# Kernel tuning notes

Measured on AMD Instinct MI355X. Metric: run time of the kernel, lower is better.

The kernel has to match this reference:

```python
import jax, jax.numpy as jnp
import numpy as np

B, N, D = 4, 10000, 64
C, E = 2, 160000  # adj channels, edges per (graph, channel)
EPS = 1e-10


def setup_inputs() -> dict:
    key = jax.random.key(0)
    k1, k2, k3 = jax.random.split(key, 3)
    inputs = jax.random.normal(k1, (B, N, D), dtype=jnp.float32)
    edge_idx = jax.random.randint(k2, (B, C, E, 2), 0, N, dtype=jnp.int32)
    weight_a = 0.1 * jax.random.normal(k3, (C, 2 * D, 1), dtype=jnp.float32)
    return {"inputs": inputs, "edge_idx": edge_idx, "weight_a": weight_a}


def _gat_channel(x, idx, wa):
    # x: [N, D], idx: [E, 2] (col 0 = scatter/dst node, col 1 = gather/src node), wa: [2D, 1]
    n = x.shape[0]
    a1 = x[idx[:, 1]]                      # [E, D]
    a2 = x[idx[:, 0]]                      # [E, D]
    score = jnp.concatenate([a1, a2], axis=1) @ wa   # [E, 1]
    e = jnp.exp(jax.nn.leaky_relu(score, negative_slope=0.2))  # [E, 1]
    denom = jax.ops.segment_sum(e, idx[:, 0], num_segments=n)  # [N, 1]  (ii @ e)
    denom_e = denom[idx[:, 1]]             # [E, 1]  (faithful to original: gather by idx[:,1])
    alpha = e / (denom_e + EPS)            # [E, 1]
    r = jax.ops.segment_sum(alpha * a1, idx[:, 0], num_segments=n)  # [N, D]
    return jax.nn.sigmoid(r)


def _gat_graph(x, idx_all, weight_a):
    # x: [N, D], idx_all: [C, E, 2], weight_a: [C, 2D, 1]
    per_ch = jax.vmap(_gat_channel, in_axes=(None, 0, 0))(x, idx_all, weight_a)  # [C, N, D]
    return per_ch.sum(axis=0)


def reference(inputs, edge_idx, weight_a):
    # inputs: [B, N, D], edge_idx: [B, C, E, 2], weight_a: [C, 2D, 1]
    return jax.vmap(_gat_graph, in_axes=(0, 0, None))(inputs, edge_idx, weight_a)
```

## Files before the change

### kernel.cpp

```cpp
#include <hip/hip_runtime.h>

#define B_ 4
#define N_ 10000
#define D_ 64
#define C_ 2
#define E_ 160000
#define BC_ (B_ * C_)
#define SH2_ 7
#define NB2_ 128
#define G2_ 79
#define CAPF_ 2560
#define NBLK_ 125
#define EPT_ 5
#define EPB_ (256 * EPT_)
#define YBLK_ (BC_ * 40)
#define POISON_ 0xAAAAAAAAu
#define EPS_ 1e-10f

__global__ void gat_yb(const float* __restrict__ x, const float* __restrict__ wa,
                       float* __restrict__ y1, float* __restrict__ y0,
                       const int* __restrict__ eidx, int* __restrict__ gcount,
                       unsigned int* __restrict__ bpack) {
    int tid = threadIdx.x;
    if (blockIdx.x < YBLK_) {
        int bc = blockIdx.x & 7;
        int n  = (blockIdx.x >> 3) * 256 + tid;
        if (n >= N_) return;
        int b = bc / C_, c = bc % C_;
        const float4* xr = (const float4*)(x + ((size_t)b * N_ + n) * D_);
        const float4* w1 = (const float4*)(wa + (size_t)c * 2 * D_);
        const float4* w0 = w1 + D_ / 4;
        float a = 0.f, bb = 0.f;
#pragma unroll
        for (int i = 0; i < D_ / 4; ++i) {
            float4 xv = xr[i];
            float4 u = w1[i], v = w0[i];
            a  += xv.x * u.x + xv.y * u.y + xv.z * u.z + xv.w * u.w;
            bb += xv.x * v.x + xv.y * v.y + xv.z * v.z + xv.w * v.w;
        }
        y1[bc * N_ + n] = a;
        y0[bc * N_ + n] = bb;
        return;
    }
    int bid = blockIdx.x - YBLK_;
    int bc  = bid & 7;
    int blk = bid >> 3;
    const int2* ep = (const int2*)eidx + (size_t)bc * E_ + (size_t)blk * EPB_;
    __shared__ int sd[128];
    __shared__ int excl[G2_], cur[G2_], gbase[G2_];
    __shared__ unsigned int stage[EPB_];
    if (tid < 128) sd[tid] = 0;
    __syncthreads();
    unsigned int pk[EPT_];
    int gg[EPT_];
#pragma unroll
    for (int k = 0; k < EPT_; ++k) {
        int2 v = ep[k * 256 + tid];
        int g  = v.x >> SH2_;
        gg[k]  = g;
        pk[k]  = ((unsigned int)g << 21) |
                 ((unsigned int)(v.x & (NB2_ - 1)) << 14) |
                 (unsigned int)v.y;
        atomicAdd(&sd[g], 1);
    }
    __syncthreads();
    int cnt = (tid < 128) ? sd[tid] : 0;
    for (int off = 1; off < 128; off <<= 1) {
        int t = (tid < 128 && tid >= off) ? sd[tid - off] : 0;
        __syncthreads();
        if (tid < 128) sd[tid] += t;
        __syncthreads();
    }
    if (tid < G2_) {
        int ex = sd[tid] - cnt;
        excl[tid]  = ex;
        cur[tid]   = ex;
        unsigned int ret = (unsigned int)atomicAdd(&gcount[bc * G2_ + tid], cnt);
        gbase[tid] = (int)(ret - POISON_);
    }
    __syncthreads();
#pragma unroll
    for (int k = 0; k < EPT_; ++k) {
        int slot = atomicAdd(&cur[gg[k]], 1);
        stage[slot] = pk[k];
    }
    __syncthreads();
#pragma unroll
    for (int k = 0; k < EPT_; ++k) {
        int idx = k * 256 + tid;
        unsigned int p = stage[idx];
        int g     = p >> 21;
        int local = idx - excl[g];
        bpack[((size_t)bc * G2_ + g) * CAPF_ + gbase[g] + local] =
            (((p >> 14) & 127u) << 16) | (p & 16383u);
    }
}

__global__ void gat_fine(const unsigned int* __restrict__ bpack,
                         const int* __restrict__ gcount,
                         const float* __restrict__ y1, const float* __restrict__ y0,
                         unsigned short* __restrict__ csr_i1,
                         int* __restrict__ rs_s, int* __restrict__ rs_e,
                         float2* __restrict__ yrd) {
    int bc = blockIdx.x & 7;
    int g  = blockIdx.x >> 3;
    int K  = (int)((unsigned int)gcount[bc * G2_ + g] - POISON_);
    int R  = (bc * G2_ + g) * CAPF_;
    const unsigned int* bp = bpack + R;
    const float* y1p = y1 + bc * N_;
    int tid = threadIdx.x;

    __shared__ int   cnt[NB2_], excl[NB2_], cur[NB2_], sd[NB2_];
    __shared__ float y0l[NB2_], den[NB2_];

    int node = g * NB2_ + tid;
    if (tid < NB2_) {
        cnt[tid] = 0;
        den[tid] = 0.f;
        y0l[tid] = (node < N_) ? y0[bc * N_ + node] : 0.f;
    }
    __syncthreads();

    for (int j = tid; j < K; j += 256) {
        unsigned int p = bp[j];
        int ln = p >> 16;
        int i1 = p & 0xffff;
        float sc = y1p[i1] + y0l[ln];
        float ev = __expf(sc > 0.f ? sc : 0.2f * sc);
        atomicAdd(&cnt[ln], 1);
        atomicAdd(&den[ln], ev);
    }
    __syncthreads();

    int v = 0;
    if (tid < NB2_) { v = cnt[tid]; sd[tid] = v; }
    __syncthreads();
    for (int off = 1; off < NB2_; off <<= 1) {
        int t = (tid < NB2_ && tid >= off) ? sd[tid - off] : 0;
        __syncthreads();
        if (tid < NB2_) sd[tid] += t;
        __syncthreads();
    }
    if (tid < NB2_) {
        int ex = sd[tid] - v;
        excl[tid] = ex;
        cur[tid]  = ex;
        if (node < N_) {
            rs_s[bc * N_ + node] = R + ex;
            rs_e[bc * N_ + node] = R + ex + v;
            yrd[bc * N_ + node]  = make_float2(y1p[node], 1.f / (den[tid] + EPS_));
        }
    }
    __syncthreads();

    for (int j = tid; j < K; j += 256) {
        unsigned int p = bp[j];
        int slot = atomicAdd(&cur[p >> 16], 1);
        csr_i1[R + slot] = (unsigned short)(p & 0xffff);
    }
}

__global__ void gat_acc(const float* __restrict__ x, const int* __restrict__ rs_s,
                        const int* __restrict__ rs_e,
                        const unsigned short* __restrict__ csr_i1,
                        const float2* __restrict__ yrd, const float* __restrict__ y0,
                        float* __restrict__ out) {
    int lane = threadIdx.x & 63;
    int w    = threadIdx.x >> 6;
    int b    = blockIdx.x & 3;
    int gp   = blockIdx.x >> 2;
    int c    = w & 1;
    int n0   = gp * 8 + (w >> 1) * 4;
    int bc   = b * C_ + c;
    const float* xb = x + (size_t)b * N_ * D_ + lane;
    const float2* yrdp = yrd + bc * N_;
    int4   sv  = *(const int4*)(rs_s + bc * N_ + n0);
    int4   ev  = *(const int4*)(rs_e + bc * N_ + n0);
    float4 y04 = *(const float4*)(y0 + bc * N_ + n0);
    int s0 = sv.x;
    int e0 = ev.x, e1 = ev.y, e2 = ev.z, e3 = ev.w;
    __shared__ float2 meta[4][64];
    float acc0 = 0.f, acc1 = 0.f, acc2 = 0.f, acc3 = 0.f;

    int pa = 0; float2 pyr = make_float2(0.f, 0.f);
    {
        int idx = s0 + lane;
        if (idx < e3) { pa = csr_i1[idx]; pyr = yrdp[pa]; }
    }
    for (int base = s0; base < e3; base += 64) {
        int idx = base + lane;
        float wgt = 0.f;
        if (idx < e3) {
            float yn = idx < e0 ? y04.x : idx < e1 ? y04.y : idx < e2 ? y04.z : y04.w;
            float sc = pyr.x + yn;
            wgt = __expf(sc > 0.f ? sc : 0.2f * sc) * pyr.y;
        }
        meta[w][lane] = make_float2(__int_as_float(pa), wgt);
        int na = 0; float2 nyr = make_float2(0.f, 0.f);
        int nidx = base + 64 + lane;
        if (base + 64 < e3 && nidx < e3) { na = csr_i1[nidx]; nyr = yrdp[na]; }
        int hi = (base + 64 < e3) ? base + 64 : e3;
#define ACC_NODE(SK, EK, ACCK)                                                \
        {                                                                     \
            int lo = (SK > base) ? SK : base;                                 \
            int h  = (EK < hi) ? EK : hi;                                     \
            int j  = lo;                                                      \
            for (; j + 4 <= h; j += 4) {                                      \
                float2 m0 = meta[w][j - base];                                \
                float2 m1 = meta[w][j - base + 1];                            \
                float2 m2 = meta[w][j - base + 2];                            \
                float2 m3 = meta[w][j - base + 3];                            \
                float x0 = xb[__float_as_int(m0.x) * D_];                     \
                float x1 = xb[__float_as_int(m1.x) * D_];                     \
                float x2 = xb[__float_as_int(m2.x) * D_];                     \
                float x3 = xb[__float_as_int(m3.x) * D_];                     \
                ACCK += m0.y * x0;                                            \
                ACCK += m1.y * x1;                                            \
                ACCK += m2.y * x2;                                            \
                ACCK += m3.y * x3;                                            \
            }                                                                 \
            for (; j < h; ++j) {                                              \
                float2 mm = meta[w][j - base];                                \
                ACCK += mm.y * xb[__float_as_int(mm.x) * D_];                 \
            }                                                                 \
        }
        ACC_NODE(s0, e0, acc0)
        ACC_NODE(e0, e1, acc1)
        ACC_NODE(e1, e2, acc2)
        ACC_NODE(e2, e3, acc3)
#undef ACC_NODE
        pa = na; pyr = nyr;
    }
    float4 sg;
    sg.x = 1.f / (1.f + __expf(-acc0));
    sg.y = 1.f / (1.f + __expf(-acc1));
    sg.z = 1.f / (1.f + __expf(-acc2));
    sg.w = 1.f / (1.f + __expf(-acc3));
    __shared__ float sh[2][4][64];
    if (c == 1) {
        sh[w >> 1][0][lane] = sg.x;
        sh[w >> 1][1][lane] = sg.y;
        sh[w >> 1][2][lane] = sg.z;
        sh[w >> 1][3][lane] = sg.w;
    }
    __syncthreads();
    if (c == 0) {
        int h = w >> 1;
        out[((size_t)b * N_ + n0 + 0) * D_ + lane] = sg.x + sh[h][0][lane];
        out[((size_t)b * N_ + n0 + 1) * D_ + lane] = sg.y + sh[h][1][lane];
        out[((size_t)b * N_ + n0 + 2) * D_ + lane] = sg.z + sh[h][2][lane];
        out[((size_t)b * N_ + n0 + 3) * D_ + lane] = sg.w + sh[h][3][lane];
    }
}

extern "C" void kernel_launch(void* const* d_in, const int* in_sizes, int n_in,
                              void* d_out, int out_size, void* d_ws, size_t ws_size,
                              hipStream_t stream) {
    const float* x    = (const float*)d_in[0];
    const int*   eidx = (const int*)d_in[1];
    const float* wa   = (const float*)d_in[2];
    float* out = (float*)d_out;

    int*    gcount = (int*)d_ws;
    float*  y1     = (float*)d_ws + 2048;
    float*  y0     = y1 + BC_ * N_;
    float2* yrd    = (float2*)(y0 + BC_ * N_);
    int*    rs_s   = (int*)(yrd + BC_ * N_);
    int*    rs_e   = rs_s + BC_ * N_;
    unsigned int* bpack = (unsigned int*)(rs_e + BC_ * N_);
    unsigned short* csr_i1 = (unsigned short*)(bpack + (size_t)BC_ * G2_ * CAPF_);

    gat_yb  <<<YBLK_ + BC_ * NBLK_, 256, 0, stream>>>(x, wa, y1, y0, eidx, gcount, bpack);
    gat_fine<<<BC_ * G2_,           256, 0, stream>>>(bpack, gcount, y1, y0,
                                                      csr_i1, rs_s, rs_e, yrd);
    gat_acc <<<B_ * N_ / 8,         256, 0, stream>>>(x, rs_s, rs_e, csr_i1, yrd, y0, out);
}
```

Before: 127.5 us.

## Use wavefront shuffle scans, vectorized edge loads, and fused per-graph projection

```diff
diff --git a/kernel.cpp b/kernel.cpp
--- a/kernel.cpp
+++ b/kernel.cpp
@@ -11,9 +11,8 @@
 #define G2_ 79
 #define CAPF_ 2560
 #define NBLK_ 125
-#define EPT_ 5
-#define EPB_ (256 * EPT_)
-#define YBLK_ (BC_ * 40)
+#define EPB_ 1280
+#define YBLK_ (B_ * 40)
 #define POISON_ 0xAAAAAAAAu
 #define EPS_ 1e-10f
 
@@ -23,54 +22,77 @@
                        unsigned int* __restrict__ bpack) {
     int tid = threadIdx.x;
     if (blockIdx.x < YBLK_) {
-        int bc = blockIdx.x & 7;
-        int n  = (blockIdx.x >> 3) * 256 + tid;
+        int b = blockIdx.x & 3;
+        int n = (blockIdx.x >> 2) * 256 + tid;
         if (n >= N_) return;
-        int b = bc / C_, c = bc % C_;
         const float4* xr = (const float4*)(x + ((size_t)b * N_ + n) * D_);
-        const float4* w1 = (const float4*)(wa + (size_t)c * 2 * D_);
-        const float4* w0 = w1 + D_ / 4;
-        float a = 0.f, bb = 0.f;
+        const float4* wp = (const float4*)wa;
+        float a0 = 0.f, b0 = 0.f, a1 = 0.f, b1 = 0.f;
 #pragma unroll
         for (int i = 0; i < D_ / 4; ++i) {
             float4 xv = xr[i];
-            float4 u = w1[i], v = w0[i];
-            a  += xv.x * u.x + xv.y * u.y + xv.z * u.z + xv.w * u.w;
-            bb += xv.x * v.x + xv.y * v.y + xv.z * v.z + xv.w * v.w;
-        }
-        y1[bc * N_ + n] = a;
-        y0[bc * N_ + n] = bb;
+            float4 u0 = wp[i], v0 = wp[i + 16];
+            float4 u1 = wp[i + 32], v1 = wp[i + 48];
+            a0 += xv.x * u0.x + xv.y * u0.y + xv.z * u0.z + xv.w * u0.w;
+            b0 += xv.x * v0.x + xv.y * v0.y + xv.z * v0.z + xv.w * v0.w;
+            a1 += xv.x * u1.x + xv.y * u1.y + xv.z * u1.z + xv.w * u1.w;
+            b1 += xv.x * v1.x + xv.y * v1.y + xv.z * v1.z + xv.w * v1.w;
+        }
+        int bc0 = b * C_;
+        y1[bc0 * N_ + n] = a0;
+        y0[bc0 * N_ + n] = b0;
+        y1[(bc0 + 1) * N_ + n] = a1;
+        y0[(bc0 + 1) * N_ + n] = b1;
         return;
     }
     int bid = blockIdx.x - YBLK_;
     int bc  = bid & 7;
     int blk = bid >> 3;
-    const int2* ep = (const int2*)eidx + (size_t)bc * E_ + (size_t)blk * EPB_;
+    const int4* ep4 = (const int4*)((const int2*)eidx + (size_t)bc * E_ +
+                                    (size_t)blk * EPB_);
     __shared__ int sd[128];
     __shared__ int excl[G2_], cur[G2_], gbase[G2_];
     __shared__ unsigned int stage[EPB_];
     if (tid < 128) sd[tid] = 0;
     __syncthreads();
-    unsigned int pk[EPT_];
-    int gg[EPT_];
+    int ne = (tid < 128) ? 6 : 4;
+    unsigned int pk[6];
+    int gg[6];
+    {
+        int4 q = ep4[tid];
+        gg[0] = q.x >> SH2_;
+        pk[0] = ((unsigned int)gg[0] << 21) | ((unsigned int)(q.x & 127) << 14) | (unsigned int)q.y;
+        gg[1] = q.z >> SH2_;
+        pk[1] = ((unsigned int)gg[1] << 21) | ((unsigned int)(q.z & 127) << 14) | (unsigned int)q.w;
+        q = ep4[tid + 256];
+        gg[2] = q.x >> SH2_;
+        pk[2] = ((unsigned int)gg[2] << 21) | ((unsigned int)(q.x & 127) << 14) | (unsigned int)q.y;
+        gg[3] = q.z >> SH2_;
+        pk[3] = ((unsigned int)gg[3] << 21) | ((unsigned int)(q.z & 127) << 14) | (unsigned int)q.w;
+        if (tid < 128) {
+            q = ep4[tid + 512];
+            gg[4] = q.x >> SH2_;
+            pk[4] = ((unsigned int)gg[4] << 21) | ((unsigned int)(q.x & 127) << 14) | (unsigned int)q.y;
+            gg[5] = q.z >> SH2_;
+            pk[5] = ((unsigned int)gg[5] << 21) | ((unsigned int)(q.z & 127) << 14) | (unsigned int)q.w;
+        }
+    }
+    for (int k = 0; k < ne; ++k) atomicAdd(&sd[gg[k]], 1);
+    __syncthreads();
+    int cnt = (tid < 128) ? sd[tid] : 0;
+    __syncthreads();
+    if (tid < 64) {
+        int v0 = sd[2 * tid], v1 = sd[2 * tid + 1];
+        int s = v0 + v1;
 #pragma unroll
-    for (int k = 0; k < EPT_; ++k) {
-        int2 v = ep[k * 256 + tid];
-        int g  = v.x >> SH2_;
-        gg[k]  = g;
-        pk[k]  = ((unsigned int)g << 21) |
-                 ((unsigned int)(v.x & (NB2_ - 1)) << 14) |
-                 (unsigned int)v.y;
-        atomicAdd(&sd[g], 1);
-    }
-    __syncthreads();
-    int cnt = (tid < 128) ? sd[tid] : 0;
-    for (int off = 1; off < 128; off <<= 1) {
-        int t = (tid < 128 && tid >= off) ? sd[tid - off] : 0;
-        __syncthreads();
-        if (tid < 128) sd[tid] += t;
-        __syncthreads();
-    }
+        for (int off = 1; off < 64; off <<= 1) {
+            int t = __shfl_up(s, off);
+            if (tid >= off) s += t;
+        }
+        sd[2 * tid]     = s - v1;
+        sd[2 * tid + 1] = s;
+    }
+    __syncthreads();
     if (tid < G2_) {
         int ex = sd[tid] - cnt;
         excl[tid]  = ex;
@@ -79,14 +101,13 @@
         gbase[tid] = (int)(ret - POISON_);
     }
     __syncthreads();
-#pragma unroll
-    for (int k = 0; k < EPT_; ++k) {
+    for (int k = 0; k < ne; ++k) {
         int slot = atomicAdd(&cur[gg[k]], 1);
         stage[slot] = pk[k];
     }
     __syncthreads();
 #pragma unroll
-    for (int k = 0; k < EPT_; ++k) {
+    for (int k = 0; k < 5; ++k) {
         int idx = k * 256 + tid;
         unsigned int p = stage[idx];
         int g     = p >> 21;
@@ -110,7 +131,7 @@
     const float* y1p = y1 + bc * N_;
     int tid = threadIdx.x;
 
-    __shared__ int   cnt[NB2_], excl[NB2_], cur[NB2_], sd[NB2_];
+    __shared__ int   cnt[NB2_], sd[NB2_], cur[NB2_];
     __shared__ float y0l[NB2_], den[NB2_];
 
     int node = g * NB2_ + tid;
@@ -132,19 +153,22 @@
     }
     __syncthreads();
 
-    int v = 0;
-    if (tid < NB2_) { v = cnt[tid]; sd[tid] = v; }
-    __syncthreads();
-    for (int off = 1; off < NB2_; off <<= 1) {
-        int t = (tid < NB2_ && tid >= off) ? sd[tid - off] : 0;
-        __syncthreads();
-        if (tid < NB2_) sd[tid] += t;
-        __syncthreads();
-    }
+    if (tid < 64) {
+        int v0 = cnt[2 * tid], v1 = cnt[2 * tid + 1];
+        int s = v0 + v1;
+#pragma unroll
+        for (int off = 1; off < 64; off <<= 1) {
+            int t = __shfl_up(s, off);
+            if (tid >= off) s += t;
+        }
+        sd[2 * tid]     = s - v1;
+        sd[2 * tid + 1] = s;
+    }
+    __syncthreads();
     if (tid < NB2_) {
+        int v  = cnt[tid];
         int ex = sd[tid] - v;
-        excl[tid] = ex;
-        cur[tid]  = ex;
+        cur[tid] = ex;
         if (node < N_) {
             rs_s[bc * N_ + node] = R + ex;
             rs_e[bc * N_ + node] = R + ex + v;
```

Result: faster. 123.8 us (-3.0%).
